# Kernel optimization log

Hardware: AMD Instinct MI355X
Metric: run time of the kernel (lower is better)

## Reference

```python
import jax, jax.numpy as jnp
import numpy as np


def _batch_pairwise_dist(x, y):
    # x: [B, Nx, D] (gts), y: [B, Ny, D] (preds) -> P: [B, Nx, Ny] squared L2
    rx = jnp.sum(x * x, axis=-1)  # [B, Nx]
    ry = jnp.sum(y * y, axis=-1)  # [B, Ny]
    zz = jnp.einsum('bnd,bmd->bnm', x, y)  # [B, Nx, Ny]
    return rx[:, :, None] + ry[:, None, :] - 2.0 * zz


def setup_inputs() -> dict:
    key = jax.random.key(0)
    k1, k2, k3 = jax.random.split(key, 3)
    B, Ngt, Npred, D = 4, 4096, 4096, 3
    preds = jax.random.normal(k1, (B, Npred, D), dtype=jnp.float32)
    gts = jax.random.normal(k2, (B, Ngt, D), dtype=jnp.float32)
    mask = jax.random.randint(k3, (B, Ngt), 0, 2).astype(jnp.bool_)
    return {"preds": preds, "gts": gts, "mask": mask}


def reference(preds, gts, mask):
    # P[b, i, j] = ||gts[b,i] - preds[b,j]||^2
    P = _batch_pairwise_dist(gts, preds)  # [B, Ngt, Npred]
    # Directional term 1: for each pred point, min over VALID gt points.
    P_masked = jnp.where(mask[:, :, None], P, jnp.inf)  # invalid gt rows -> +inf
    loss_1 = jnp.sum(jnp.min(P_masked, axis=1))
    # Directional term 2: for each VALID gt point, min over all pred points.
    mins_gt = jnp.min(P, axis=2)  # [B, Ngt]
    loss_2 = jnp.sum(jnp.where(mask, mins_gt, 0.0))
    return loss_1 + loss_2
```

## Files before the change

kernel.cpp:

```cpp
#include <hip/hip_runtime.h>

#define NBATCH 4
#define NPTS   4096
#define XPT    8
#define XCHUNK (256 * XPT)
#define NXC    (NPTS / XCHUNK)
#define YCHUNK 128
#define NYC    (NPTS / YCHUNK)
#define BIGF   1e30f

__global__ __launch_bounds__(256)
void chamfer_min_kernel(const float* __restrict__ preds,
                        const float* __restrict__ gts,
                        const int* __restrict__ mask,
                        float* __restrict__ partial,
                        float* __restrict__ out) {
    const int zc  = blockIdx.z;
    const int dir = zc >> 2;
    const int b   = zc & 3;
    const int tid = threadIdx.x;

    if ((zc | blockIdx.x | blockIdx.y | tid) == 0) out[0] = 0.0f;

    const float* X = (dir == 0 ? preds : gts) + (size_t)b * NPTS * 3;
    const float* Y = (dir == 0 ? gts : preds) + (size_t)b * NPTS * 3;

    __shared__ float4 sy[YCHUNK];
    const int cbase = blockIdx.y * YCHUNK;
    if (tid < YCHUNK) {
        const int j = cbase + tid;
        const float y0 = Y[j * 3 + 0];
        const float y1 = Y[j * 3 + 1];
        const float y2 = Y[j * 3 + 2];
        float ry = y0 * y0 + y1 * y1 + y2 * y2;
        if (dir == 0 && mask[b * NPTS + j] == 0) ry = BIGF;
        sy[tid] = make_float4(y0, y1, y2, ry);
    }
    __syncthreads();

    float a0[XPT], a1[XPT], a2[XPT], rx[XPT], m[XPT];
    const int xbase = blockIdx.x * XCHUNK + tid;
    #pragma unroll
    for (int i = 0; i < XPT; ++i) {
        const int x = xbase + i * 256;
        float v0 = X[x * 3 + 0], v1 = X[x * 3 + 1], v2 = X[x * 3 + 2];
        rx[i] = v0 * v0 + v1 * v1 + v2 * v2;
        a0[i] = -2.0f * v0; a1[i] = -2.0f * v1; a2[i] = -2.0f * v2;
        m[i] = BIGF;
    }

    #pragma unroll 2
    for (int k = 0; k < YCHUNK; k += 4) {
        const float4 p0 = sy[k + 0];
        const float4 p1 = sy[k + 1];
        const float4 p2 = sy[k + 2];
        const float4 p3 = sy[k + 3];
        #pragma unroll
        for (int i = 0; i < XPT; ++i) {
            const float t0 = fmaf(a0[i], p0.x, fmaf(a1[i], p0.y, fmaf(a2[i], p0.z, p0.w)));
            const float t1 = fmaf(a0[i], p1.x, fmaf(a1[i], p1.y, fmaf(a2[i], p1.z, p1.w)));
            const float t2 = fmaf(a0[i], p2.x, fmaf(a1[i], p2.y, fmaf(a2[i], p2.z, p2.w)));
            const float t3 = fmaf(a0[i], p3.x, fmaf(a1[i], p3.y, fmaf(a2[i], p3.z, p3.w)));
            m[i] = fminf(fminf(m[i], t0), t1);
            m[i] = fminf(fminf(m[i], t2), t3);
        }
    }

    float* prow = partial + ((size_t)(dir * NBATCH + b) * NYC + blockIdx.y) * NPTS
                + blockIdx.x * XCHUNK + tid;
    #pragma unroll
    for (int i = 0; i < XPT; ++i)
        prow[i * 256] = rx[i] + m[i];
}

__global__ __launch_bounds__(256)
void chamfer_reduce_kernel(const float* __restrict__ partial,
                           const int* __restrict__ mask,
                           float* __restrict__ out) {
    const int gid = blockIdx.x * blockDim.x + threadIdx.x;
    const int h   = gid & 1;
    const int p   = gid >> 1;
    const int dir = p >> 14;
    const int b   = (p >> 12) & 3;
    const int x   = p & 4095;

    const float* base = partial + ((size_t)(dir * NBATCH + b) * NYC) * NPTS + x
                      + (size_t)(h * 16) * NPTS;
    float m = base[0];
    #pragma unroll
    for (int c = 1; c < 16; ++c) m = fminf(m, base[(size_t)c * NPTS]);

    m = fminf(m, __shfl_xor(m, 1, 64));

    float v = 0.0f;
    if (h == 0) {
        v = m;
        if (dir == 1 && mask[b * NPTS + x] == 0) v = 0.0f;
    }

    #pragma unroll
    for (int off = 32; off > 0; off >>= 1)
        v += __shfl_down(v, off, 64);

    __shared__ float wsum[4];
    const int wave = threadIdx.x >> 6;
    if ((threadIdx.x & 63) == 0) wsum[wave] = v;
    __syncthreads();
    if (threadIdx.x == 0)
        atomicAdd(out, wsum[0] + wsum[1] + wsum[2] + wsum[3]);
}

extern "C" void kernel_launch(void* const* d_in, const int* in_sizes, int n_in,
                              void* d_out, int out_size, void* d_ws, size_t ws_size,
                              hipStream_t stream) {
    const float* preds = (const float*)d_in[0];
    const float* gts   = (const float*)d_in[1];
    const int*   mask  = (const int*)d_in[2];
    float* out = (float*)d_out;

    float* partial = (float*)d_ws;

    dim3 grid(NXC, NYC, 2 * NBATCH);
    chamfer_min_kernel<<<grid, 256, 0, stream>>>(preds, gts, mask, partial, out);

    chamfer_reduce_kernel<<<2 * (2 * NBATCH * NPTS) / 256, 256, 0, stream>>>(
        partial, mask, out);
}
```

Baseline: 22.88 us.

## Fuse chamfer min and reduction into one pass with flag-based final sum

Replaces the two-kernel scheme (partial mins written to workspace, then a separate reduce kernel) with a single kernel. Each block loads all 4096 Y points into LDS, handles 64 X points with four waves splitting the Y range, and combines the four wave minima in shared memory. Each block publishes its sum through release/acquire flags, and block 0 spins on those flags to form the final total. This removes the second launch and the partial-buffer traffic, but each thread now holds one X point instead of eight, so it gets less register reuse and more LDS reads per FMA. The spin-wait in block 0 also assumes block 0 stays resident while the other blocks run, and it relies on the flags in the workspace starting at zero.

```diff
diff --git a/kernel.cpp b/kernel.cpp
--- a/kernel.cpp
+++ b/kernel.cpp
@@ -2,112 +2,109 @@
 
 #define NBATCH 4
 #define NPTS   4096
-#define XPT    8
-#define XCHUNK (256 * XPT)
-#define NXC    (NPTS / XCHUNK)
-#define YCHUNK 128
-#define NYC    (NPTS / YCHUNK)
+#define XCB    64
+#define NXB    (NPTS / XCB)
+#define NBLK   (2 * NBATCH * NXB)
+#define YSPLIT 4
+#define YLEN   (NPTS / YSPLIT)
 #define BIGF   1e30f
 
-__global__ __launch_bounds__(256)
-void chamfer_min_kernel(const float* __restrict__ preds,
-                        const float* __restrict__ gts,
-                        const int* __restrict__ mask,
-                        float* __restrict__ partial,
-                        float* __restrict__ out) {
-    const int zc  = blockIdx.z;
+__global__ __launch_bounds__(256, 2)
+void chamfer_onepass_kernel(const float* __restrict__ preds,
+                            const float* __restrict__ gts,
+                            const int* __restrict__ mask,
+                            float* __restrict__ blocksum,
+                            unsigned* __restrict__ flags,
+                            float* __restrict__ out) {
+    const int bid = blockIdx.x;
+    const int tid = threadIdx.x;
+    const int zc  = bid >> 6;
+    const int xc  = bid & (NXB - 1);
     const int dir = zc >> 2;
     const int b   = zc & 3;
-    const int tid = threadIdx.x;
-
-    if ((zc | blockIdx.x | blockIdx.y | tid) == 0) out[0] = 0.0f;
 
     const float* X = (dir == 0 ? preds : gts) + (size_t)b * NPTS * 3;
     const float* Y = (dir == 0 ? gts : preds) + (size_t)b * NPTS * 3;
 
-    __shared__ float4 sy[YCHUNK];
-    const int cbase = blockIdx.y * YCHUNK;
-    if (tid < YCHUNK) {
-        const int j = cbase + tid;
-        const float y0 = Y[j * 3 + 0];
-        const float y1 = Y[j * 3 + 1];
-        const float y2 = Y[j * 3 + 2];
+    __shared__ float4 sy[NPTS];
+    for (int t = tid; t < NPTS; t += 256) {
+        const float y0 = Y[t * 3 + 0];
+        const float y1 = Y[t * 3 + 1];
+        const float y2 = Y[t * 3 + 2];
         float ry = y0 * y0 + y1 * y1 + y2 * y2;
-        if (dir == 0 && mask[b * NPTS + j] == 0) ry = BIGF;
-        sy[tid] = make_float4(y0, y1, y2, ry);
+        if (dir == 0 && mask[b * NPTS + t] == 0) ry = BIGF;
+        sy[t] = make_float4(y0, y1, y2, ry);
     }
+
+    const int lx = tid & 63;
+    const int q  = tid >> 6;
+    const int x  = xc * XCB + lx;
+    const float v0 = X[x * 3 + 0], v1 = X[x * 3 + 1], v2 = X[x * 3 + 2];
+    const float rx = v0 * v0 + v1 * v1 + v2 * v2;
+    const float a0 = -2.0f * v0, a1 = -2.0f * v1, a2 = -2.0f * v2;
+
     __syncthreads();
 
-    float a0[XPT], a1[XPT], a2[XPT], rx[XPT], m[XPT];
-    const int xbase = blockIdx.x * XCHUNK + tid;
-    #pragma unroll
-    for (int i = 0; i < XPT; ++i) {
-        const int x = xbase + i * 256;
-        float v0 = X[x * 3 + 0], v1 = X[x * 3 + 1], v2 = X[x * 3 + 2];
-        rx[i] = v0 * v0 + v1 * v1 + v2 * v2;
-        a0[i] = -2.0f * v0; a1[i] = -2.0f * v1; a2[i] = -2.0f * v2;
-        m[i] = BIGF;
-    }
-
+    float m = BIGF;
+    const int kbeg = q * YLEN;
     #pragma unroll 2
-    for (int k = 0; k < YCHUNK; k += 4) {
+    for (int k = kbeg; k < kbeg + YLEN; k += 4) {
         const float4 p0 = sy[k + 0];
         const float4 p1 = sy[k + 1];
         const float4 p2 = sy[k + 2];
         const float4 p3 = sy[k + 3];
+        const float t0 = fmaf(a0, p0.x, fmaf(a1, p0.y, fmaf(a2, p0.z, p0.w)));
+        const float t1 = fmaf(a0, p1.x, fmaf(a1, p1.y, fmaf(a2, p1.z, p1.w)));
+        const float t2 = fmaf(a0, p2.x, fmaf(a1, p2.y, fmaf(a2, p2.z, p2.w)));
+        const float t3 = fmaf(a0, p3.x, fmaf(a1, p3.y, fmaf(a2, p3.z, p3.w)));
+        m = fminf(fminf(m, t0), t1);
+        m = fminf(fminf(m, t2), t3);
+    }
+
+    __shared__ float sm[YSPLIT][XCB];
+    sm[q][lx] = m;
+    __syncthreads();
+
+    if (q == 0) {
+        const float mm = fminf(fminf(sm[0][lx], sm[1][lx]),
+                               fminf(sm[2][lx], sm[3][lx]));
+        float val = rx + mm;
+        if (dir == 1 && mask[b * NPTS + x] == 0) val = 0.0f;
+
         #pragma unroll
-        for (int i = 0; i < XPT; ++i) {
-            const float t0 = fmaf(a0[i], p0.x, fmaf(a1[i], p0.y, fmaf(a2[i], p0.z, p0.w)));
-            const float t1 = fmaf(a0[i], p1.x, fmaf(a1[i], p1.y, fmaf(a2[i], p1.z, p1.w)));
-            const float t2 = fmaf(a0[i], p2.x, fmaf(a1[i], p2.y, fmaf(a2[i], p2.z, p2.w)));
-            const float t3 = fmaf(a0[i], p3.x, fmaf(a1[i], p3.y, fmaf(a2[i], p3.z, p3.w)));
-            m[i] = fminf(fminf(m[i], t0), t1);
-            m[i] = fminf(fminf(m[i], t2), t3);
+        for (int off = 32; off > 0; off >>= 1)
+            val += __shfl_down(val, off, 64);
+
+        if (lx == 0) {
+            __hip_atomic_store(&blocksum[bid], val, __ATOMIC_RELAXED,
+                               __HIP_MEMORY_SCOPE_AGENT);
+            __hip_atomic_store(&flags[bid], 1u, __ATOMIC_RELEASE,
+                               __HIP_MEMORY_SCOPE_AGENT);
         }
     }
 
-    float* prow = partial + ((size_t)(dir * NBATCH + b) * NYC + blockIdx.y) * NPTS
-                + blockIdx.x * XCHUNK + tid;
-    #pragma unroll
-    for (int i = 0; i < XPT; ++i)
-        prow[i * 256] = rx[i] + m[i];
-}
+    if (bid == 0) {
+        float acc = 0.0f;
+        #pragma unroll
+        for (int r = 0; r < NBLK / 256; ++r) {
+            const int i = r * 256 + tid;
+            while (__hip_atomic_load(&flags[i], __ATOMIC_ACQUIRE,
+                                     __HIP_MEMORY_SCOPE_AGENT) != 1u) {}
+            acc += __hip_atomic_load(&blocksum[i], __ATOMIC_RELAXED,
+                                     __HIP_MEMORY_SCOPE_AGENT);
+            __hip_atomic_store(&flags[i], 0u, __ATOMIC_RELAXED,
+                               __HIP_MEMORY_SCOPE_AGENT);
+        }
+        #pragma unroll
+        for (int off = 32; off > 0; off >>= 1)
+            acc += __shfl_down(acc, off, 64);
 
-__global__ __launch_bounds__(256)
-void chamfer_reduce_kernel(const float* __restrict__ partial,
-                           const int* __restrict__ mask,
-                           float* __restrict__ out) {
-    const int gid = blockIdx.x * blockDim.x + threadIdx.x;
-    const int h   = gid & 1;
-    const int p   = gid >> 1;
-    const int dir = p >> 14;
-    const int b   = (p >> 12) & 3;
-    const int x   = p & 4095;
-
-    const float* base = partial + ((size_t)(dir * NBATCH + b) * NYC) * NPTS + x
-                      + (size_t)(h * 16) * NPTS;
-    float m = base[0];
-    #pragma unroll
-    for (int c = 1; c < 16; ++c) m = fminf(m, base[(size_t)c * NPTS]);
-
-    m = fminf(m, __shfl_xor(m, 1, 64));
-
-    float v = 0.0f;
-    if (h == 0) {
-        v = m;
-        if (dir == 1 && mask[b * NPTS + x] == 0) v = 0.0f;
+        __shared__ float ws4[4];
+        if ((tid & 63) == 0) ws4[tid >> 6] = acc;
+        __syncthreads();
+        if (tid == 0)
+            out[0] = ws4[0] + ws4[1] + ws4[2] + ws4[3];
     }
-
-    #pragma unroll
-    for (int off = 32; off > 0; off >>= 1)
-        v += __shfl_down(v, off, 64);
-
-    __shared__ float wsum[4];
-    const int wave = threadIdx.x >> 6;
-    if ((threadIdx.x & 63) == 0) wsum[wave] = v;
-    __syncthreads();
-    if (threadIdx.x == 0)
-        atomicAdd(out, wsum[0] + wsum[1] + wsum[2] + wsum[3]);
 }
 
 extern "C" void kernel_launch(void* const* d_in, const int* in_sizes, int n_in,
@@ -118,11 +115,9 @@
     const int*   mask  = (const int*)d_in[2];
     float* out = (float*)d_out;
 
-    float* partial = (float*)d_ws;
+    float*    blocksum = (float*)d_ws;
+    unsigned* flags    = (unsigned*)(blocksum + NBLK);
 
-    dim3 grid(NXC, NYC, 2 * NBATCH);
-    chamfer_min_kernel<<<grid, 256, 0, stream>>>(preds, gts, mask, partial, out);
-
-    chamfer_reduce_kernel<<<2 * (2 * NBATCH * NPTS) / 256, 256, 0, stream>>>(
-        partial, mask, out);
+    chamfer_onepass_kernel<<<NBLK, 256, 0, stream>>>(
+        preds, gts, mask, blocksum, flags, out);
 }
```

Result: slower. 28.95 us (+26.5%).

## Fuse min and reduce kernels into one launch with flag-based inter-block sync

Applied to the files above, without the earlier changes.

Merges the pairwise-min kernel and the reduction kernel into a single 512-block launch. Blocks publish per-chunk partial minima with release flags. The yc==0 blocks spin-wait on those flags, reduce their column, and publish a per-slice sum. Block 0 then waits for the 16 slice sums and writes the final output without atomics. This removes a second kernel launch and the out-zeroing atomic path. In exchange it relies on all 512 blocks being co-resident, since the spin-waits can deadlock otherwise, and it puts the final reduction on a serialized critical path.

```diff
diff --git a/kernel.cpp b/kernel.cpp
--- a/kernel.cpp
+++ b/kernel.cpp
@@ -3,32 +3,39 @@
 #define NBATCH 4
 #define NPTS   4096
 #define XPT    8
-#define XCHUNK (256 * XPT)
-#define NXC    (NPTS / XCHUNK)
+#define XCHUNK 2048
+#define NXC    2
 #define YCHUNK 128
-#define NYC    (NPTS / YCHUNK)
+#define NYC    32
+#define NBLK   512
 #define BIGF   1e30f
 
+#define LOAD_AG(p)    __hip_atomic_load((p),  __ATOMIC_RELAXED, __HIP_MEMORY_SCOPE_AGENT)
+#define STORE_AG(p,v) __hip_atomic_store((p),(v), __ATOMIC_RELAXED, __HIP_MEMORY_SCOPE_AGENT)
+
 __global__ __launch_bounds__(256)
-void chamfer_min_kernel(const float* __restrict__ preds,
-                        const float* __restrict__ gts,
-                        const int* __restrict__ mask,
-                        float* __restrict__ partial,
-                        float* __restrict__ out) {
-    const int zc  = blockIdx.z;
+void chamfer_fused_kernel(const float* __restrict__ preds,
+                          const float* __restrict__ gts,
+                          const int* __restrict__ mask,
+                          float* __restrict__ partial,
+                          float* __restrict__ rsum,
+                          unsigned* __restrict__ flag1,
+                          unsigned* __restrict__ flag2,
+                          float* __restrict__ out) {
+    const int bid = blockIdx.x;
+    const int tid = threadIdx.x;
+    const int xc  = bid & 1;
+    const int yc  = (bid >> 1) & 31;
+    const int zc  = bid >> 6;
     const int dir = zc >> 2;
     const int b   = zc & 3;
-    const int tid = threadIdx.x;
-
-    if ((zc | blockIdx.x | blockIdx.y | tid) == 0) out[0] = 0.0f;
 
     const float* X = (dir == 0 ? preds : gts) + (size_t)b * NPTS * 3;
     const float* Y = (dir == 0 ? gts : preds) + (size_t)b * NPTS * 3;
 
     __shared__ float4 sy[YCHUNK];
-    const int cbase = blockIdx.y * YCHUNK;
     if (tid < YCHUNK) {
-        const int j = cbase + tid;
+        const int j = yc * YCHUNK + tid;
         const float y0 = Y[j * 3 + 0];
         const float y1 = Y[j * 3 + 1];
         const float y2 = Y[j * 3 + 2];
@@ -36,10 +43,9 @@
         if (dir == 0 && mask[b * NPTS + j] == 0) ry = BIGF;
         sy[tid] = make_float4(y0, y1, y2, ry);
     }
-    __syncthreads();
 
     float a0[XPT], a1[XPT], a2[XPT], rx[XPT], m[XPT];
-    const int xbase = blockIdx.x * XCHUNK + tid;
+    const int xbase = xc * XCHUNK + tid;
     #pragma unroll
     for (int i = 0; i < XPT; ++i) {
         const int x = xbase + i * 256;
@@ -48,6 +54,7 @@
         a0[i] = -2.0f * v0; a1[i] = -2.0f * v1; a2[i] = -2.0f * v2;
         m[i] = BIGF;
     }
+    __syncthreads();
 
     #pragma unroll 2
     for (int k = 0; k < YCHUNK; k += 4) {
@@ -66,48 +73,69 @@
         }
     }
 
-    float* prow = partial + ((size_t)(dir * NBATCH + b) * NYC + blockIdx.y) * NPTS
-                + blockIdx.x * XCHUNK + tid;
-    #pragma unroll
-    for (int i = 0; i < XPT; ++i)
-        prow[i * 256] = rx[i] + m[i];
-}
+    {
+        float* prow = partial + ((size_t)zc * NYC + yc) * NPTS + xbase;
+        #pragma unroll
+        for (int i = 0; i < XPT; ++i)
+            STORE_AG(prow + i * 256, rx[i] + m[i]);
+    }
+    __syncthreads();
+    if (tid == 0)
+        __hip_atomic_store(&flag1[bid], 1u, __ATOMIC_RELEASE,
+                           __HIP_MEMORY_SCOPE_AGENT);
 
-__global__ __launch_bounds__(256)
-void chamfer_reduce_kernel(const float* __restrict__ partial,
-                           const int* __restrict__ mask,
-                           float* __restrict__ out) {
-    const int gid = blockIdx.x * blockDim.x + threadIdx.x;
-    const int h   = gid & 1;
-    const int p   = gid >> 1;
-    const int dir = p >> 14;
-    const int b   = (p >> 12) & 3;
-    const int x   = p & 4095;
+    if (yc == 0) {
+        if (tid < NYC) {
+            while (LOAD_AG(&flag1[bid + 2 * tid]) != 1u)
+                __builtin_amdgcn_s_sleep(8);
+        }
+        __syncthreads();
+        __threadfence();
 
-    const float* base = partial + ((size_t)(dir * NBATCH + b) * NYC) * NPTS + x
-                      + (size_t)(h * 16) * NPTS;
-    float m = base[0];
-    #pragma unroll
-    for (int c = 1; c < 16; ++c) m = fminf(m, base[(size_t)c * NPTS]);
+        float acc = 0.0f;
+        #pragma unroll
+        for (int i = 0; i < XPT; ++i) {
+            const int x = xbase + i * 256;
+            const float* col = partial + (size_t)zc * NYC * NPTS + x;
+            float mm = LOAD_AG(col);
+            #pragma unroll
+            for (int r = 1; r < NYC; ++r)
+                mm = fminf(mm, LOAD_AG(col + (size_t)r * NPTS));
+            float v = mm;
+            if (dir == 1 && mask[b * NPTS + x] == 0) v = 0.0f;
+            acc += v;
+        }
+        #pragma unroll
+        for (int off = 32; off > 0; off >>= 1)
+            acc += __shfl_down(acc, off, 64);
 
-    m = fminf(m, __shfl_xor(m, 1, 64));
+        __shared__ float ws4[4];
+        if ((tid & 63) == 0) ws4[tid >> 6] = acc;
+        __syncthreads();
 
-    float v = 0.0f;
-    if (h == 0) {
-        v = m;
-        if (dir == 1 && mask[b * NPTS + x] == 0) v = 0.0f;
+        const int ridx = zc * 2 + xc;
+        if (tid == 0) {
+            STORE_AG(&rsum[ridx], ws4[0] + ws4[1] + ws4[2] + ws4[3]);
+            __hip_atomic_store(&flag2[ridx], 1u, __ATOMIC_RELEASE,
+                               __HIP_MEMORY_SCOPE_AGENT);
+        }
+        if (tid < NYC)
+            STORE_AG(&flag1[bid + 2 * tid], 0u);
     }
 
-    #pragma unroll
-    for (int off = 32; off > 0; off >>= 1)
-        v += __shfl_down(v, off, 64);
-
-    __shared__ float wsum[4];
-    const int wave = threadIdx.x >> 6;
-    if ((threadIdx.x & 63) == 0) wsum[wave] = v;
-    __syncthreads();
-    if (threadIdx.x == 0)
-        atomicAdd(out, wsum[0] + wsum[1] + wsum[2] + wsum[3]);
+    if (bid == 0) {
+        float v = 0.0f;
+        if (tid < 16) {
+            while (LOAD_AG(&flag2[tid]) != 1u)
+                __builtin_amdgcn_s_sleep(8);
+            v = LOAD_AG(&rsum[tid]);
+        }
+        #pragma unroll
+        for (int off = 8; off > 0; off >>= 1)
+            v += __shfl_down(v, off, 16);
+        if (tid == 0) out[0] = v;
+        if (tid < 16) STORE_AG(&flag2[tid], 0u);
+    }
 }
 
 extern "C" void kernel_launch(void* const* d_in, const int* in_sizes, int n_in,
@@ -118,11 +146,11 @@
     const int*   mask  = (const int*)d_in[2];
     float* out = (float*)d_out;
 
-    float* partial = (float*)d_ws;
+    float*    partial = (float*)d_ws;
+    float*    rsum    = partial + (size_t)8 * NYC * NPTS;
+    unsigned* flag1   = (unsigned*)(rsum + 16);
+    unsigned* flag2   = flag1 + NBLK;
 
-    dim3 grid(NXC, NYC, 2 * NBATCH);
-    chamfer_min_kernel<<<grid, 256, 0, stream>>>(preds, gts, mask, partial, out);
-
-    chamfer_reduce_kernel<<<2 * (2 * NBATCH * NPTS) / 256, 256, 0, stream>>>(
-        partial, mask, out);
+    chamfer_fused_kernel<<<NBLK, 256, 0, stream>>>(
+        preds, gts, mask, partial, rsum, flag1, flag2, out);
 }
```

Measured after the change: 42.51 us. +85.8%, slower.

## Use packed FP32 FMA over paired Y points and vectorize reduce kernel

Applied to the files above, without the earlier changes.

Rearranges the shared-memory Y tile into structure-of-arrays pairs so the inner distance loop can issue packed two-wide FP32 FMAs (v_pk_fma_f32) and halve FMA instruction count. It also moves the barrier after the X register setup so global loads overlap, and rewrites the reduction kernel so each thread reduces four adjacent columns across all 32 Y-chunks with float4 loads and an int4 mask load. The cost is extra packing work and fewer reduce threads, each with a longer serial chain.

```diff
diff --git a/kernel.cpp b/kernel.cpp
--- a/kernel.cpp
+++ b/kernel.cpp
@@ -6,8 +6,11 @@
 #define XCHUNK (256 * XPT)
 #define NXC    (NPTS / XCHUNK)
 #define YCHUNK 128
+#define NPAIR  (YCHUNK / 2)
 #define NYC    (NPTS / YCHUNK)
 #define BIGF   1e30f
+
+typedef float v2f __attribute__((ext_vector_type(2)));
 
 __global__ __launch_bounds__(256)
 void chamfer_min_kernel(const float* __restrict__ preds,
@@ -25,49 +28,55 @@
     const float* X = (dir == 0 ? preds : gts) + (size_t)b * NPTS * 3;
     const float* Y = (dir == 0 ? gts : preds) + (size_t)b * NPTS * 3;
 
-    __shared__ float4 sy[YCHUNK];
+    __shared__ float4 sp[2 * NPAIR];
     const int cbase = blockIdx.y * YCHUNK;
-    if (tid < YCHUNK) {
-        const int j = cbase + tid;
-        const float y0 = Y[j * 3 + 0];
-        const float y1 = Y[j * 3 + 1];
-        const float y2 = Y[j * 3 + 2];
-        float ry = y0 * y0 + y1 * y1 + y2 * y2;
-        if (dir == 0 && mask[b * NPTS + j] == 0) ry = BIGF;
-        sy[tid] = make_float4(y0, y1, y2, ry);
+    if (tid < NPAIR) {
+        const int ja = cbase + 2 * tid;
+        const int jb = ja + 1;
+        const float xa = Y[ja * 3 + 0], ya = Y[ja * 3 + 1], za = Y[ja * 3 + 2];
+        const float xb = Y[jb * 3 + 0], yb = Y[jb * 3 + 1], zb = Y[jb * 3 + 2];
+        float ra = xa * xa + ya * ya + za * za;
+        float rb = xb * xb + yb * yb + zb * zb;
+        if (dir == 0) {
+            if (mask[b * NPTS + ja] == 0) ra = BIGF;
+            if (mask[b * NPTS + jb] == 0) rb = BIGF;
+        }
+        sp[2 * tid + 0] = make_float4(xa, xb, ya, yb);
+        sp[2 * tid + 1] = make_float4(za, zb, ra, rb);
     }
-    __syncthreads();
 
-    float a0[XPT], a1[XPT], a2[XPT], rx[XPT], m[XPT];
+    v2f A0[XPT], A1[XPT], A2[XPT];
+    float rx[XPT], m[XPT];
     const int xbase = blockIdx.x * XCHUNK + tid;
     #pragma unroll
     for (int i = 0; i < XPT; ++i) {
         const int x = xbase + i * 256;
-        float v0 = X[x * 3 + 0], v1 = X[x * 3 + 1], v2 = X[x * 3 + 2];
+        const float v0 = X[x * 3 + 0], v1 = X[x * 3 + 1], v2 = X[x * 3 + 2];
         rx[i] = v0 * v0 + v1 * v1 + v2 * v2;
-        a0[i] = -2.0f * v0; a1[i] = -2.0f * v1; a2[i] = -2.0f * v2;
+        const float s0 = -2.0f * v0, s1 = -2.0f * v1, s2 = -2.0f * v2;
+        A0[i] = (v2f){s0, s0}; A1[i] = (v2f){s1, s1}; A2[i] = (v2f){s2, s2};
         m[i] = BIGF;
     }
+    __syncthreads();
 
     #pragma unroll 2
-    for (int k = 0; k < YCHUNK; k += 4) {
-        const float4 p0 = sy[k + 0];
-        const float4 p1 = sy[k + 1];
-        const float4 p2 = sy[k + 2];
-        const float4 p3 = sy[k + 3];
+    for (int j = 0; j < NPAIR; ++j) {
+        const float4 E0 = sp[2 * j + 0];
+        const float4 E1 = sp[2 * j + 1];
+        const v2f X2 = (v2f){E0.x, E0.y};
+        const v2f Y2 = (v2f){E0.z, E0.w};
+        const v2f Z2 = (v2f){E1.x, E1.y};
+        const v2f R2 = (v2f){E1.z, E1.w};
         #pragma unroll
         for (int i = 0; i < XPT; ++i) {
-            const float t0 = fmaf(a0[i], p0.x, fmaf(a1[i], p0.y, fmaf(a2[i], p0.z, p0.w)));
-            const float t1 = fmaf(a0[i], p1.x, fmaf(a1[i], p1.y, fmaf(a2[i], p1.z, p1.w)));
-            const float t2 = fmaf(a0[i], p2.x, fmaf(a1[i], p2.y, fmaf(a2[i], p2.z, p2.w)));
-            const float t3 = fmaf(a0[i], p3.x, fmaf(a1[i], p3.y, fmaf(a2[i], p3.z, p3.w)));
-            m[i] = fminf(fminf(m[i], t0), t1);
-            m[i] = fminf(fminf(m[i], t2), t3);
+            v2f t = __builtin_elementwise_fma(A2[i], Z2, R2);
+            t = __builtin_elementwise_fma(A1[i], Y2, t);
+            t = __builtin_elementwise_fma(A0[i], X2, t);
+            m[i] = fminf(fminf(m[i], t.x), t.y);
         }
     }
 
-    float* prow = partial + ((size_t)(dir * NBATCH + b) * NYC + blockIdx.y) * NPTS
-                + blockIdx.x * XCHUNK + tid;
+    float* prow = partial + ((size_t)zc * NYC + blockIdx.y) * NPTS + xbase;
     #pragma unroll
     for (int i = 0; i < XPT; ++i)
         prow[i * 256] = rx[i] + m[i];
@@ -78,33 +87,36 @@
                            const int* __restrict__ mask,
                            float* __restrict__ out) {
     const int gid = blockIdx.x * blockDim.x + threadIdx.x;
-    const int h   = gid & 1;
-    const int p   = gid >> 1;
-    const int dir = p >> 14;
-    const int b   = (p >> 12) & 3;
-    const int x   = p & 4095;
+    const int p4  = gid * 4;
+    const int dir = p4 >> 14;
+    const int b   = (p4 >> 12) & 3;
+    const int x   = p4 & 4095;
+    const int zc  = dir * NBATCH + b;
 
-    const float* base = partial + ((size_t)(dir * NBATCH + b) * NYC) * NPTS + x
-                      + (size_t)(h * 16) * NPTS;
-    float m = base[0];
+    const float4* base = (const float4*)(partial + (size_t)zc * NYC * NPTS + x);
+    float4 m4 = base[0];
     #pragma unroll
-    for (int c = 1; c < 16; ++c) m = fminf(m, base[(size_t)c * NPTS]);
+    for (int r = 1; r < NYC; ++r) {
+        const float4 v = base[(size_t)r * (NPTS / 4)];
+        m4.x = fminf(m4.x, v.x); m4.y = fminf(m4.y, v.y);
+        m4.z = fminf(m4.z, v.z); m4.w = fminf(m4.w, v.w);
+    }
 
-    m = fminf(m, __shfl_xor(m, 1, 64));
-
-    float v = 0.0f;
-    if (h == 0) {
-        v = m;
-        if (dir == 1 && mask[b * NPTS + x] == 0) v = 0.0f;
+    float acc;
+    if (dir == 1) {
+        const int4 mk = *(const int4*)(mask + b * NPTS + x);
+        acc = (mk.x ? m4.x : 0.0f) + (mk.y ? m4.y : 0.0f)
+            + (mk.z ? m4.z : 0.0f) + (mk.w ? m4.w : 0.0f);
+    } else {
+        acc = m4.x + m4.y + m4.z + m4.w;
     }
 
     #pragma unroll
     for (int off = 32; off > 0; off >>= 1)
-        v += __shfl_down(v, off, 64);
+        acc += __shfl_down(acc, off, 64);
 
     __shared__ float wsum[4];
-    const int wave = threadIdx.x >> 6;
-    if ((threadIdx.x & 63) == 0) wsum[wave] = v;
+    if ((threadIdx.x & 63) == 0) wsum[threadIdx.x >> 6] = acc;
     __syncthreads();
     if (threadIdx.x == 0)
         atomicAdd(out, wsum[0] + wsum[1] + wsum[2] + wsum[3]);
@@ -123,6 +135,6 @@
     dim3 grid(NXC, NYC, 2 * NBATCH);
     chamfer_min_kernel<<<grid, 256, 0, stream>>>(preds, gts, mask, partial, out);
 
-    chamfer_reduce_kernel<<<2 * (2 * NBATCH * NPTS) / 256, 256, 0, stream>>>(
+    chamfer_reduce_kernel<<<(2 * NBATCH * NPTS / 4) / 256, 256, 0, stream>>>(
         partial, mask, out);
 }
```

New measurement: 21.31 us. 1.07x faster.
